# Kernel optimization log

Hardware: AMD Instinct MI355X
Metric: run time of the kernel (lower is better)

## Reference

```python
import jax, jax.numpy as jnp
import numpy as np


def setup_inputs() -> dict:
    key = jax.random.key(0)
    k1, k2 = jax.random.split(key)
    B, D = 8192, 256
    z1 = jax.random.normal(k1, (B, D), dtype=jnp.float32)
    z2 = jax.random.normal(k2, (B, D), dtype=jnp.float32)
    temperature = 0.1
    logit_scale = jnp.asarray(np.log(1.0 / temperature), dtype=jnp.float32)
    return {"z1": z1, "z2": z2, "logit_scale": logit_scale}


def reference(z1, z2, logit_scale):
    B = z1.shape[0]
    z = jnp.concatenate([z1, z2], axis=0)            # [2B, D]
    scale = jnp.minimum(jnp.exp(logit_scale), 100.0)
    logits = jnp.matmul(z, z.T) * scale              # [2B, 2B]
    N = 2 * B
    eye = jnp.eye(N, dtype=bool)
    logits = jnp.where(eye, jnp.float32(-1e9), logits)
    targets = jnp.concatenate([jnp.arange(B, 2 * B), jnp.arange(0, B)], axis=0)
    logp = jax.nn.log_softmax(logits, axis=-1)       # stable single-pass
    nll = -jnp.take_along_axis(logp, targets[:, None], axis=-1)[:, 0]
    return jnp.mean(nll)
```

## Files before the change

kernel.cpp:

```cpp
#include <hip/hip_runtime.h>
#include <hip/hip_bf16.h>

#define N_TOT 16384
#define B_HALF 8192
#define D 256
#define NGRAN 32
#define BN 32
#define NSPLIT 8
#define COLS_PER_SPLIT (N_TOT / NSPLIT)
#define NTILES (COLS_PER_SPLIT / BN)
#define NWAVE 8
#define BM (NWAVE * 64)

#define LOG2E 1.4426950408889634f
#define LN2   0.6931471805599453f

typedef short bf16x8 __attribute__((ext_vector_type(8)));
typedef float f32x4 __attribute__((ext_vector_type(4)));

__device__ __forceinline__ float fexp2(float x) {
#if __has_builtin(__builtin_amdgcn_exp2f)
    return __builtin_amdgcn_exp2f(x);
#else
    return __expf(x * LN2);
#endif
}

__device__ __forceinline__ ushort f2bf(float x) {
    uint32_t u = __float_as_uint(x);
    uint32_t r = u + 0x7FFFu + ((u >> 16) & 1u);
    return (ushort)(r >> 16);
}

__global__ void convert_kernel(const float* __restrict__ z1,
                               const float* __restrict__ z2,
                               const float* __restrict__ lsp,
                               ushort* __restrict__ zt) {
    const float scale = fminf(__expf(lsp[0]), 100.0f);
    const float s = __fsqrt_rn(scale * LOG2E);
    int T = blockIdx.x * blockDim.x + threadIdx.x;
    const int c = T >> 14;
    const int r = T & (N_TOT - 1);
    const int half_elems = B_HALF * D;
    int e = r * D + c * 8;
    const float* src = (e < half_elems) ? (z1 + e) : (z2 + (e - half_elems));
    float4 f0 = *reinterpret_cast<const float4*>(src);
    float4 f1 = *reinterpret_cast<const float4*>(src + 4);
    ushort o[8];
    o[0] = f2bf(f0.x * s); o[1] = f2bf(f0.y * s); o[2] = f2bf(f0.z * s); o[3] = f2bf(f0.w * s);
    o[4] = f2bf(f1.x * s); o[5] = f2bf(f1.y * s); o[6] = f2bf(f1.z * s); o[7] = f2bf(f1.w * s);
    *reinterpret_cast<bf16x8*>(zt + (size_t)T * 8) = *reinterpret_cast<bf16x8*>(o);
}

__global__ void target_kernel(const float* __restrict__ z1,
                              const float* __restrict__ z2,
                              const float* __restrict__ lsp,
                              float* __restrict__ tnat) {
    const int r    = blockIdx.x * 4 + (threadIdx.x >> 6);
    const int lane = threadIdx.x & 63;
    const float* zr = (r < B_HALF) ? (z1 + (size_t)r * D) : (z2 + (size_t)(r - B_HALF) * D);
    const float* zp = (r < B_HALF) ? (z2 + (size_t)r * D) : (z1 + (size_t)(r - B_HALF) * D);
    float4 a = *reinterpret_cast<const float4*>(zr + lane * 4);
    float4 b = *reinterpret_cast<const float4*>(zp + lane * 4);
    float d = a.x * b.x + a.y * b.y + a.z * b.z + a.w * b.w;
#pragma unroll
    for (int off = 1; off < 64; off <<= 1) d += __shfl_xor(d, off);
    if (lane == 0) {
        const float scale = fminf(__expf(lsp[0]), 100.0f);
        tnat[r] = scale * d;
    }
}

template<bool MASKD>
__device__ __forceinline__ void epilogue(const f32x4 (&acc)[4][2],
                                         float (&m2)[16], float (&l2)[16],
                                         int qrow0, int crow0, int g, int lg) {
#pragma unroll
    for (int mi = 0; mi < 4; ++mi) {
#pragma unroll
        for (int j = 0; j < 4; ++j) {
            const int slot = mi * 4 + j;
            float v0 = acc[mi][0][j], v1 = acc[mi][1][j];
            if (MASKD) {
                const int r  = qrow0 + mi * 16 + g * 4 + j;
                const int c0 = crow0 + lg;
                if (c0      == r) v0 = -1e30f;
                if (c0 + 16 == r) v1 = -1e30f;
            }
            const float m_old = m2[slot];
            float m_new = fmaxf(fmaxf(v0, v1), m_old);
            float er = fexp2(m_old - m_new);
            float e0 = fexp2(v0 - m_new);
            float e1 = fexp2(v1 - m_new);
            l2[slot] = __builtin_fmaf(l2[slot], er, e0 + e1);
            m2[slot] = m_new;
        }
    }
}

__global__ __launch_bounds__(512)
__attribute__((amdgpu_waves_per_eu(2, 2)))
void infonce_main(const ushort* __restrict__ zt,
                  float* __restrict__ part) {
    __shared__ ushort ks[NWAVE][BN * NGRAN * 8];

    const int tid  = threadIdx.x;
    const int wid  = tid >> 6;
    const int lane = tid & 63;
    const int g    = lane >> 4;
    const int lg   = lane & 15;
    const int qrow0   = blockIdx.y * BM + wid * 64;
    const int split   = blockIdx.x;
    const int colbase = split * COLS_PER_SPLIT;

    bf16x8 afrag[4][8];
#pragma unroll
    for (int kk = 0; kk < 8; ++kk)
#pragma unroll
        for (int mi = 0; mi < 4; ++mi)
            afrag[mi][kk] = *reinterpret_cast<const bf16x8*>(
                zt + ((size_t)(kk * 4 + g) * N_TOT + qrow0 + mi * 16 + lg) * 8);

    float m2[16], l2[16];
#pragma unroll
    for (int s = 0; s < 16; ++s) { m2[s] = -1e30f; l2[s] = 0.0f; }

    const ushort* srcW = zt + ((size_t)(lane >> 5) * N_TOT + (lane & 31)) * 8;

#define STAGE(t)                                                                     \
    {                                                                                \
        const ushort* s_ = srcW + (size_t)(colbase + (t) * BN) * 8;                  \
        _Pragma("unroll")                                                            \
        for (int it = 0; it < 16; ++it)                                              \
            __builtin_amdgcn_global_load_lds(                                        \
                (const __attribute__((address_space(1))) void*)(s_ + (size_t)it * 2 * N_TOT * 8), \
                (__attribute__((address_space(3))) void*)&ks[wid][it * 512],         \
                16, 0, 0);                                                           \
    }

    if (wid & 4) __builtin_amdgcn_s_sleep(19);

    STAGE(0);

    const char* kb = (const char*)(&ks[wid][0]) + g * 512 + lg * 16;

    for (int t = 0; t < NTILES; ++t) {
        asm volatile("s_waitcnt vmcnt(0)" ::: "memory");
        __builtin_amdgcn_sched_barrier(0);

        f32x4 acc[4][2];
#pragma unroll
        for (int mi = 0; mi < 4; ++mi)
#pragma unroll
            for (int n = 0; n < 2; ++n) acc[mi][n] = (f32x4){0.f, 0.f, 0.f, 0.f};

#pragma unroll
        for (int kk = 0; kk < 8; ++kk) {
#pragma unroll
            for (int n = 0; n < 2; ++n) {
                bf16x8 b = *reinterpret_cast<const bf16x8*>(kb + kk * 2048 + n * 256);
                acc[0][n] = __builtin_amdgcn_mfma_f32_16x16x32_bf16(afrag[0][kk], b, acc[0][n], 0, 0, 0);
                acc[1][n] = __builtin_amdgcn_mfma_f32_16x16x32_bf16(afrag[1][kk], b, acc[1][n], 0, 0, 0);
                acc[2][n] = __builtin_amdgcn_mfma_f32_16x16x32_bf16(afrag[2][kk], b, acc[2][n], 0, 0, 0);
                acc[3][n] = __builtin_amdgcn_mfma_f32_16x16x32_bf16(afrag[3][kk], b, acc[3][n], 0, 0, 0);
            }
        }

        asm volatile("s_waitcnt lgkmcnt(0)" ::: "memory");
        __builtin_amdgcn_sched_barrier(0);
        if (t + 1 < NTILES) STAGE(t + 1);

        const int crow0 = colbase + t * BN;
        if ((crow0 >> 6) == (qrow0 >> 6))
            epilogue<true >(acc, m2, l2, qrow0, crow0, g, lg);
        else
            epilogue<false>(acc, m2, l2, qrow0, crow0, g, lg);
    }
#undef STAGE

#pragma unroll
    for (int s = 0; s < 16; ++s) {
        float m = m2[s], l = l2[s];
#pragma unroll
        for (int off = 1; off < 16; off <<= 1) {
            float mo = __shfl_xor(m, off);
            float lo = __shfl_xor(l, off);
            float mm = fmaxf(m, mo);
            l = l * fexp2(m - mm) + lo * fexp2(mo - mm);
            m = mm;
        }
        m2[s] = m; l2[s] = l;
    }
    if (lg == 0) {
#pragma unroll
        for (int mi = 0; mi < 4; ++mi)
#pragma unroll
            for (int j = 0; j < 4; ++j) {
                int r = qrow0 + mi * 16 + g * 4 + j;
                int s = mi * 4 + j;
                float* p = part + (size_t)(r * NSPLIT + split) * 2;
                p[0] = m2[s]; p[1] = l2[s];
            }
    }
}

__global__ void reduce_kernel(const float* __restrict__ part,
                              const float* __restrict__ tnat,
                              float* __restrict__ bsum) {
    int r = blockIdx.x * 256 + threadIdx.x;
    float m = -1e30f, l = 0.f;
#pragma unroll
    for (int s = 0; s < NSPLIT; ++s) {
        const float* p = part + (size_t)(r * NSPLIT + s) * 2;
        float ms = p[0], lv = p[1];
        float mm = fmaxf(m, ms);
        l = l * fexp2(m - mm) + lv * fexp2(ms - mm);
        m = mm;
    }
    float v = LN2 * (m + __log2f(l)) - tnat[r];
#pragma unroll
    for (int off = 1; off < 64; off <<= 1) v += __shfl_xor(v, off);
    __shared__ float ws4[4];
    int lane = threadIdx.x & 63, wid = threadIdx.x >> 6;
    if (lane == 0) ws4[wid] = v;
    __syncthreads();
    if (threadIdx.x == 0)
        bsum[blockIdx.x] = ws4[0] + ws4[1] + ws4[2] + ws4[3];
}

__global__ void final_kernel(const float* __restrict__ bsum,
                             float* __restrict__ out) {
    float v = bsum[threadIdx.x];
#pragma unroll
    for (int off = 1; off < 64; off <<= 1) v += __shfl_xor(v, off);
    if (threadIdx.x == 0) out[0] = v * (1.0f / (float)N_TOT);
}

extern "C" void kernel_launch(void* const* d_in, const int* in_sizes, int n_in,
                              void* d_out, int out_size, void* d_ws, size_t ws_size,
                              hipStream_t stream) {
    const float* z1 = (const float*)d_in[0];
    const float* z2 = (const float*)d_in[1];
    const float* ls = (const float*)d_in[2];
    float* out = (float*)d_out;

    ushort* zt   = (ushort*)d_ws;
    float*  part = (float*)((char*)d_ws + (size_t)N_TOT * D * 2);
    float*  tnat = (float*)((char*)part + (size_t)N_TOT * NSPLIT * 2 * sizeof(float));
    float*  bsum = (float*)((char*)tnat + (size_t)N_TOT * sizeof(float));

    convert_kernel<<<(N_TOT * NGRAN) / 256, 256, 0, stream>>>(z1, z2, ls, zt);
    target_kernel<<<N_TOT / 4, 256, 0, stream>>>(z1, z2, ls, tnat);
    dim3 grid(NSPLIT, N_TOT / BM);
    infonce_main<<<grid, 512, 0, stream>>>(zt, part);
    reduce_kernel<<<N_TOT / 256, 256, 0, stream>>>(part, tnat, bsum);
    final_kernel<<<1, 64, 0, stream>>>(bsum, out);
}
```

Baseline: 158.4 us.

## Software-pipeline MFMA tiles with previous tile's softmax epilogue via double accumulators

```diff
diff --git a/kernel.cpp b/kernel.cpp
--- a/kernel.cpp
+++ b/kernel.cpp
@@ -71,12 +71,12 @@
     }
 }
 
-template<bool MASKD>
-__device__ __forceinline__ void epilogue(const f32x4 (&acc)[4][2],
+template<bool MASKD, int MI0>
+__device__ __forceinline__ void epi_half(const f32x4 (&acc)[4][2],
                                          float (&m2)[16], float (&l2)[16],
                                          int qrow0, int crow0, int g, int lg) {
 #pragma unroll
-    for (int mi = 0; mi < 4; ++mi) {
+    for (int mi = MI0; mi < MI0 + 2; ++mi) {
 #pragma unroll
         for (int j = 0; j < 4; ++j) {
             const int slot = mi * 4 + j;
@@ -138,44 +138,75 @@
                 16, 0, 0);                                                           \
     }
 
-    if (wid & 4) __builtin_amdgcn_s_sleep(19);
+    const char* kb = (const char*)(&ks[wid][0]) + g * 512 + lg * 16;
+
+    f32x4 accA[4][2], accB[4][2];
+
+#define ZERO(ACC)                                                                    \
+    { _Pragma("unroll") for (int mi = 0; mi < 4; ++mi)                               \
+        _Pragma("unroll") for (int n = 0; n < 2; ++n)                                \
+            ACC[mi][n] = (f32x4){0.f, 0.f, 0.f, 0.f}; }
+
+#define MFMA_HALF(ACC, KK0)                                                          \
+    { _Pragma("unroll") for (int kk = KK0; kk < (KK0) + 4; ++kk) {                   \
+        _Pragma("unroll") for (int n = 0; n < 2; ++n) {                              \
+            bf16x8 b = *reinterpret_cast<const bf16x8*>(kb + kk * 2048 + n * 256);   \
+            ACC[0][n] = __builtin_amdgcn_mfma_f32_16x16x32_bf16(afrag[0][kk], b, ACC[0][n], 0, 0, 0); \
+            ACC[1][n] = __builtin_amdgcn_mfma_f32_16x16x32_bf16(afrag[1][kk], b, ACC[1][n], 0, 0, 0); \
+            ACC[2][n] = __builtin_amdgcn_mfma_f32_16x16x32_bf16(afrag[2][kk], b, ACC[2][n], 0, 0, 0); \
+            ACC[3][n] = __builtin_amdgcn_mfma_f32_16x16x32_bf16(afrag[3][kk], b, ACC[3][n], 0, 0, 0); \
+        } } }
+
+#define EPI_H0(ACCE, CROW)                                                           \
+    { if (((CROW) >> 6) == (qrow0 >> 6)) epi_half<true , 0>(ACCE, m2, l2, qrow0, (CROW), g, lg); \
+      else                               epi_half<false, 0>(ACCE, m2, l2, qrow0, (CROW), g, lg); }
+#define EPI_H1(ACCE, CROW)                                                           \
+    { if (((CROW) >> 6) == (qrow0 >> 6)) epi_half<true , 2>(ACCE, m2, l2, qrow0, (CROW), g, lg); \
+      else                               epi_half<false, 2>(ACCE, m2, l2, qrow0, (CROW), g, lg); }
+
+#define BODY(T, ACCW, ACCE)                                                          \
+    {                                                                                \
+        const int crow_prev = colbase + ((T) - 1) * BN;                              \
+        asm volatile("s_waitcnt vmcnt(0)" ::: "memory");        \
+        __builtin_amdgcn_sched_barrier(0);                                           \
+        ZERO(ACCW);                                                                  \
+        __builtin_amdgcn_s_setprio(1);                                               \
+        MFMA_HALF(ACCW, 0);                                                          \
+        EPI_H0(ACCE, crow_prev);                           \
+        MFMA_HALF(ACCW, 4);                                                          \
+        __builtin_amdgcn_s_setprio(0);                                               \
+        asm volatile("s_waitcnt lgkmcnt(0)" ::: "memory");        \
+        __builtin_amdgcn_sched_barrier(0);                                           \
+        if ((T) + 1 < NTILES) STAGE((T) + 1);                                        \
+        EPI_H1(ACCE, crow_prev);                            \
+    }
 
     STAGE(0);
-
-    const char* kb = (const char*)(&ks[wid][0]) + g * 512 + lg * 16;
-
-    for (int t = 0; t < NTILES; ++t) {
-        asm volatile("s_waitcnt vmcnt(0)" ::: "memory");
-        __builtin_amdgcn_sched_barrier(0);
-
-        f32x4 acc[4][2];
-#pragma unroll
-        for (int mi = 0; mi < 4; ++mi)
-#pragma unroll
-            for (int n = 0; n < 2; ++n) acc[mi][n] = (f32x4){0.f, 0.f, 0.f, 0.f};
-
-#pragma unroll
-        for (int kk = 0; kk < 8; ++kk) {
-#pragma unroll
-            for (int n = 0; n < 2; ++n) {
-                bf16x8 b = *reinterpret_cast<const bf16x8*>(kb + kk * 2048 + n * 256);
-                acc[0][n] = __builtin_amdgcn_mfma_f32_16x16x32_bf16(afrag[0][kk], b, acc[0][n], 0, 0, 0);
-                acc[1][n] = __builtin_amdgcn_mfma_f32_16x16x32_bf16(afrag[1][kk], b, acc[1][n], 0, 0, 0);
-                acc[2][n] = __builtin_amdgcn_mfma_f32_16x16x32_bf16(afrag[2][kk], b, acc[2][n], 0, 0, 0);
-                acc[3][n] = __builtin_amdgcn_mfma_f32_16x16x32_bf16(afrag[3][kk], b, acc[3][n], 0, 0, 0);
-            }
-        }
-
-        asm volatile("s_waitcnt lgkmcnt(0)" ::: "memory");
-        __builtin_amdgcn_sched_barrier(0);
-        if (t + 1 < NTILES) STAGE(t + 1);
-
-        const int crow0 = colbase + t * BN;
-        if ((crow0 >> 6) == (qrow0 >> 6))
-            epilogue<true >(acc, m2, l2, qrow0, crow0, g, lg);
-        else
-            epilogue<false>(acc, m2, l2, qrow0, crow0, g, lg);
-    }
+    asm volatile("s_waitcnt vmcnt(0)" ::: "memory");
+    __builtin_amdgcn_sched_barrier(0);
+    ZERO(accB);
+    MFMA_HALF(accB, 0);
+    MFMA_HALF(accB, 4);
+    asm volatile("s_waitcnt lgkmcnt(0)" ::: "memory");
+    __builtin_amdgcn_sched_barrier(0);
+    STAGE(1);
+
+    for (int tp = 0; tp < 31; ++tp) {
+        BODY(2 * tp + 1, accA, accB);
+        BODY(2 * tp + 2, accB, accA);
+    }
+    BODY(63, accA, accB);
+
+    {
+        const int crow_last = colbase + 63 * BN;
+        EPI_H0(accA, crow_last);
+        EPI_H1(accA, crow_last);
+    }
+#undef BODY
+#undef EPI_H0
+#undef EPI_H1
+#undef MFMA_HALF
+#undef ZERO
 #undef STAGE
 
 #pragma unroll
```

Result: slower. 168.3 us (+6.3%).

## Gate online-softmax exp updates per wave and split load wait across K halves

Applied to the files above, without the earlier changes.

```diff
diff --git a/kernel.cpp b/kernel.cpp
--- a/kernel.cpp
+++ b/kernel.cpp
@@ -14,6 +14,7 @@
 
 #define LOG2E 1.4426950408889634f
 #define LN2   0.6931471805599453f
+#define GATE_THR 30.0f
 
 typedef short bf16x8 __attribute__((ext_vector_type(8)));
 typedef float f32x4 __attribute__((ext_vector_type(4)));
@@ -72,28 +73,39 @@
 }
 
 template<bool MASKD>
-__device__ __forceinline__ void epilogue(const f32x4 (&acc)[4][2],
-                                         float (&m2)[16], float (&l2)[16],
-                                         int qrow0, int crow0, int g, int lg) {
+__device__ __forceinline__ void epilogue_g(const f32x4 (&acc)[4][2],
+                                           float (&m2)[16], float (&l2)[16],
+                                           int qrow0, int crow0, int g, int lg) {
 #pragma unroll
     for (int mi = 0; mi < 4; ++mi) {
-#pragma unroll
-        for (int j = 0; j < 4; ++j) {
-            const int slot = mi * 4 + j;
-            float v0 = acc[mi][0][j], v1 = acc[mi][1][j];
-            if (MASKD) {
-                const int r  = qrow0 + mi * 16 + g * 4 + j;
-                const int c0 = crow0 + lg;
-                if (c0      == r) v0 = -1e30f;
-                if (c0 + 16 == r) v1 = -1e30f;
-            }
-            const float m_old = m2[slot];
-            float m_new = fmaxf(fmaxf(v0, v1), m_old);
-            float er = fexp2(m_old - m_new);
-            float e0 = fexp2(v0 - m_new);
-            float e1 = fexp2(v1 - m_new);
-            l2[slot] = __builtin_fmaf(l2[slot], er, e0 + e1);
-            m2[slot] = m_new;
+        float v0[4], v1[4];
+#pragma unroll
+        for (int j = 0; j < 4; ++j) { v0[j] = acc[mi][0][j]; v1[j] = acc[mi][1][j]; }
+        if (MASKD) {
+            const int c0 = crow0 + lg;
+#pragma unroll
+            for (int j = 0; j < 4; ++j) {
+                const int r = qrow0 + mi * 16 + g * 4 + j;
+                if (c0      == r) v0[j] = -1e30f;
+                if (c0 + 16 == r) v1[j] = -1e30f;
+            }
+        }
+        const int s0 = mi * 4;
+        float gmax = fmaxf(fmaxf(fmaxf(v0[0], v1[0]), fmaxf(v0[1], v1[1])),
+                           fmaxf(fmaxf(v0[2], v1[2]), fmaxf(v0[3], v1[3])));
+        float mmin = fminf(fminf(m2[s0], m2[s0 + 1]), fminf(m2[s0 + 2], m2[s0 + 3]));
+        if (__any(gmax > mmin - GATE_THR)) {
+#pragma unroll
+            for (int j = 0; j < 4; ++j) {
+                const int slot = s0 + j;
+                const float m_old = m2[slot];
+                float m_new = fmaxf(fmaxf(v0[j], v1[j]), m_old);
+                float er = fexp2(m_old - m_new);
+                float e0 = fexp2(v0[j] - m_new);
+                float e1 = fexp2(v1[j] - m_new);
+                l2[slot] = __builtin_fmaf(l2[slot], er, e0 + e1);
+                m2[slot] = m_new;
+            }
         }
     }
 }
@@ -145,17 +157,16 @@
     const char* kb = (const char*)(&ks[wid][0]) + g * 512 + lg * 16;
 
     for (int t = 0; t < NTILES; ++t) {
-        asm volatile("s_waitcnt vmcnt(0)" ::: "memory");
+        f32x4 acc[4][2];
+#pragma unroll
+        for (int mi = 0; mi < 4; ++mi)
+#pragma unroll
+            for (int n = 0; n < 2; ++n) acc[mi][n] = (f32x4){0.f, 0.f, 0.f, 0.f};
+
+        asm volatile("s_waitcnt vmcnt(8)" ::: "memory");
         __builtin_amdgcn_sched_barrier(0);
-
-        f32x4 acc[4][2];
-#pragma unroll
-        for (int mi = 0; mi < 4; ++mi)
-#pragma unroll
-            for (int n = 0; n < 2; ++n) acc[mi][n] = (f32x4){0.f, 0.f, 0.f, 0.f};
-
-#pragma unroll
-        for (int kk = 0; kk < 8; ++kk) {
+#pragma unroll
+        for (int kk = 0; kk < 4; ++kk) {
 #pragma unroll
             for (int n = 0; n < 2; ++n) {
                 bf16x8 b = *reinterpret_cast<const bf16x8*>(kb + kk * 2048 + n * 256);
@@ -165,6 +176,19 @@
                 acc[3][n] = __builtin_amdgcn_mfma_f32_16x16x32_bf16(afrag[3][kk], b, acc[3][n], 0, 0, 0);
             }
         }
+        asm volatile("s_waitcnt vmcnt(0)" ::: "memory");
+        __builtin_amdgcn_sched_barrier(0);
+#pragma unroll
+        for (int kk = 4; kk < 8; ++kk) {
+#pragma unroll
+            for (int n = 0; n < 2; ++n) {
+                bf16x8 b = *reinterpret_cast<const bf16x8*>(kb + kk * 2048 + n * 256);
+                acc[0][n] = __builtin_amdgcn_mfma_f32_16x16x32_bf16(afrag[0][kk], b, acc[0][n], 0, 0, 0);
+                acc[1][n] = __builtin_amdgcn_mfma_f32_16x16x32_bf16(afrag[1][kk], b, acc[1][n], 0, 0, 0);
+                acc[2][n] = __builtin_amdgcn_mfma_f32_16x16x32_bf16(afrag[2][kk], b, acc[2][n], 0, 0, 0);
+                acc[3][n] = __builtin_amdgcn_mfma_f32_16x16x32_bf16(afrag[3][kk], b, acc[3][n], 0, 0, 0);
+            }
+        }
 
         asm volatile("s_waitcnt lgkmcnt(0)" ::: "memory");
         __builtin_amdgcn_sched_barrier(0);
@@ -172,9 +196,9 @@
 
         const int crow0 = colbase + t * BN;
         if ((crow0 >> 6) == (qrow0 >> 6))
-            epilogue<true >(acc, m2, l2, qrow0, crow0, g, lg);
+            epilogue_g<true >(acc, m2, l2, qrow0, crow0, g, lg);
         else
-            epilogue<false>(acc, m2, l2, qrow0, crow0, g, lg);
+            epilogue_g<false>(acc, m2, l2, qrow0, crow0, g, lg);
     }
 #undef STAGE
 
```

New measurement: 239.6 us. 1.51x slower.

## Split waves into MFMA producers and softmax consumers with shared double buffers

Applied to the files above, without the earlier changes.

```diff
diff --git a/kernel.cpp b/kernel.cpp
--- a/kernel.cpp
+++ b/kernel.cpp
@@ -6,17 +6,21 @@
 #define D 256
 #define NGRAN 32
 #define BN 32
-#define NSPLIT 8
+#define NSPLIT 4
 #define COLS_PER_SPLIT (N_TOT / NSPLIT)
-#define NTILES (COLS_PER_SPLIT / BN)
-#define NWAVE 8
-#define BM (NWAVE * 64)
+#define NT (COLS_PER_SPLIT / BN)
+#define BM 256
 
 #define LOG2E 1.4426950408889634f
 #define LN2   0.6931471805599453f
 
 typedef short bf16x8 __attribute__((ext_vector_type(8)));
 typedef float f32x4 __attribute__((ext_vector_type(4)));
+
+#define SBAR() asm volatile("s_barrier" ::: "memory")
+#define WAITV4()   { asm volatile("s_waitcnt vmcnt(4)" ::: "memory"); __builtin_amdgcn_sched_barrier(0); }
+#define WAITV0()   { asm volatile("s_waitcnt vmcnt(0)" ::: "memory"); __builtin_amdgcn_sched_barrier(0); }
+#define WAITLGKM() { asm volatile("s_waitcnt lgkmcnt(0)" ::: "memory"); __builtin_amdgcn_sched_barrier(0); }
 
 __device__ __forceinline__ float fexp2(float x) {
 #if __has_builtin(__builtin_amdgcn_exp2f)
@@ -102,105 +106,131 @@
 __attribute__((amdgpu_waves_per_eu(2, 2)))
 void infonce_main(const ushort* __restrict__ zt,
                   float* __restrict__ part) {
-    __shared__ ushort ks[NWAVE][BN * NGRAN * 8];
+    __shared__ ushort ks[2][BN * NGRAN * 8];
+    __shared__ float  accb[2][4][2048];
 
     const int tid  = threadIdx.x;
     const int wid  = tid >> 6;
     const int lane = tid & 63;
     const int g    = lane >> 4;
     const int lg   = lane & 15;
-    const int qrow0   = blockIdx.y * BM + wid * 64;
-    const int split   = blockIdx.x;
-    const int colbase = split * COLS_PER_SPLIT;
-
-    bf16x8 afrag[4][8];
-#pragma unroll
-    for (int kk = 0; kk < 8; ++kk)
-#pragma unroll
-        for (int mi = 0; mi < 4; ++mi)
-            afrag[mi][kk] = *reinterpret_cast<const bf16x8*>(
-                zt + ((size_t)(kk * 4 + g) * N_TOT + qrow0 + mi * 16 + lg) * 8);
-
-    float m2[16], l2[16];
-#pragma unroll
-    for (int s = 0; s < 16; ++s) { m2[s] = -1e30f; l2[s] = 0.0f; }
-
-    const ushort* srcW = zt + ((size_t)(lane >> 5) * N_TOT + (lane & 31)) * 8;
-
-#define STAGE(t)                                                                     \
-    {                                                                                \
-        const ushort* s_ = srcW + (size_t)(colbase + (t) * BN) * 8;                  \
-        _Pragma("unroll")                                                            \
-        for (int it = 0; it < 16; ++it)                                              \
-            __builtin_amdgcn_global_load_lds(                                        \
-                (const __attribute__((address_space(1))) void*)(s_ + (size_t)it * 2 * N_TOT * 8), \
-                (__attribute__((address_space(3))) void*)&ks[wid][it * 512],         \
-                16, 0, 0);                                                           \
-    }
-
-    if (wid & 4) __builtin_amdgcn_s_sleep(19);
-
-    STAGE(0);
-
-    const char* kb = (const char*)(&ks[wid][0]) + g * 512 + lg * 16;
-
-    for (int t = 0; t < NTILES; ++t) {
-        asm volatile("s_waitcnt vmcnt(0)" ::: "memory");
-        __builtin_amdgcn_sched_barrier(0);
-
-        f32x4 acc[4][2];
-#pragma unroll
-        for (int mi = 0; mi < 4; ++mi)
-#pragma unroll
-            for (int n = 0; n < 2; ++n) acc[mi][n] = (f32x4){0.f, 0.f, 0.f, 0.f};
-
-#pragma unroll
-        for (int kk = 0; kk < 8; ++kk) {
-#pragma unroll
-            for (int n = 0; n < 2; ++n) {
-                bf16x8 b = *reinterpret_cast<const bf16x8*>(kb + kk * 2048 + n * 256);
-                acc[0][n] = __builtin_amdgcn_mfma_f32_16x16x32_bf16(afrag[0][kk], b, acc[0][n], 0, 0, 0);
-                acc[1][n] = __builtin_amdgcn_mfma_f32_16x16x32_bf16(afrag[1][kk], b, acc[1][n], 0, 0, 0);
-                acc[2][n] = __builtin_amdgcn_mfma_f32_16x16x32_bf16(afrag[2][kk], b, acc[2][n], 0, 0, 0);
-                acc[3][n] = __builtin_amdgcn_mfma_f32_16x16x32_bf16(afrag[3][kk], b, acc[3][n], 0, 0, 0);
-            }
-        }
-
-        asm volatile("s_waitcnt lgkmcnt(0)" ::: "memory");
-        __builtin_amdgcn_sched_barrier(0);
-        if (t + 1 < NTILES) STAGE(t + 1);
-
-        const int crow0 = colbase + t * BN;
-        if ((crow0 >> 6) == (qrow0 >> 6))
-            epilogue<true >(acc, m2, l2, qrow0, crow0, g, lg);
-        else
-            epilogue<false>(acc, m2, l2, qrow0, crow0, g, lg);
-    }
+    const bool isProd = (wid < 4);
+    const int band  = isProd ? wid : (wid - 4);
+    const int qrow0 = blockIdx.y * BM + band * 64;
+    const int colbase = blockIdx.x * COLS_PER_SPLIT;
+
+    const int accoff = g * 128 + lg * 4;
+
+    if (isProd) {
+        bf16x8 afrag[4][8];
+#pragma unroll
+        for (int kk = 0; kk < 8; ++kk)
+#pragma unroll
+            for (int mi = 0; mi < 4; ++mi)
+                afrag[mi][kk] = *reinterpret_cast<const bf16x8*>(
+                    zt + ((size_t)(kk * 4 + g) * N_TOT + qrow0 + mi * 16 + lg) * 8);
+
+        const ushort* srcW = zt + ((size_t)(wid * 2 + (lane >> 5)) * N_TOT + (lane & 31)) * 8;
+        const int dstbase = (wid * 64) * 8;
+
+#define STAGE(buf, t)                                                               \
+    {                                                                               \
+        const ushort* s_ = srcW + (size_t)(colbase + (t) * BN) * 8;                 \
+        _Pragma("unroll")                                                           \
+        for (int it = 0; it < 4; ++it)                                              \
+            __builtin_amdgcn_global_load_lds(                                       \
+                (const __attribute__((address_space(1))) void*)(s_ + (size_t)it * 8 * N_TOT * 8), \
+                (__attribute__((address_space(3))) void*)&ks[buf][it * 2048 + dstbase], \
+                16, 0, 0);                                                          \
+    }
+
+        const char* kb0 = (const char*)(&ks[0][0]) + g * 512 + lg * 16;
+
+        STAGE(0, 0);
+
+        for (int t = 0; t <= NT; ++t) {
+            SBAR();
+            if (t < NT) {
+                if (t + 1 < NT) { STAGE((t + 1) & 1, t + 1); WAITV4(); }
+                else            { WAITV0(); }
+
+                f32x4 acc[4][2];
+#pragma unroll
+                for (int mi = 0; mi < 4; ++mi)
+#pragma unroll
+                    for (int n = 0; n < 2; ++n) acc[mi][n] = (f32x4){0.f, 0.f, 0.f, 0.f};
+
+                const char* kb = kb0 + ((t & 1) << 14);
+#pragma unroll
+                for (int kk = 0; kk < 8; ++kk) {
+#pragma unroll
+                    for (int n = 0; n < 2; ++n) {
+                        bf16x8 b = *reinterpret_cast<const bf16x8*>(kb + kk * 2048 + n * 256);
+                        acc[0][n] = __builtin_amdgcn_mfma_f32_16x16x32_bf16(afrag[0][kk], b, acc[0][n], 0, 0, 0);
+                        acc[1][n] = __builtin_amdgcn_mfma_f32_16x16x32_bf16(afrag[1][kk], b, acc[1][n], 0, 0, 0);
+                        acc[2][n] = __builtin_amdgcn_mfma_f32_16x16x32_bf16(afrag[2][kk], b, acc[2][n], 0, 0, 0);
+                        acc[3][n] = __builtin_amdgcn_mfma_f32_16x16x32_bf16(afrag[3][kk], b, acc[3][n], 0, 0, 0);
+                    }
+                }
+
+                float* ab = &accb[t & 1][band][0] + accoff;
+#pragma unroll
+                for (int mi = 0; mi < 4; ++mi)
+#pragma unroll
+                    for (int n = 0; n < 2; ++n)
+                        *reinterpret_cast<f32x4*>(ab + mi * 512 + n * 64) = acc[mi][n];
+                WAITLGKM();
+            }
+        }
 #undef STAGE
-
-#pragma unroll
-    for (int s = 0; s < 16; ++s) {
-        float m = m2[s], l = l2[s];
-#pragma unroll
-        for (int off = 1; off < 16; off <<= 1) {
-            float mo = __shfl_xor(m, off);
-            float lo = __shfl_xor(l, off);
-            float mm = fmaxf(m, mo);
-            l = l * fexp2(m - mm) + lo * fexp2(mo - mm);
-            m = mm;
-        }
-        m2[s] = m; l2[s] = l;
-    }
-    if (lg == 0) {
-#pragma unroll
-        for (int mi = 0; mi < 4; ++mi)
-#pragma unroll
-            for (int j = 0; j < 4; ++j) {
-                int r = qrow0 + mi * 16 + g * 4 + j;
-                int s = mi * 4 + j;
-                float* p = part + (size_t)(r * NSPLIT + split) * 2;
-                p[0] = m2[s]; p[1] = l2[s];
-            }
+    } else {
+        float m2[16], l2[16];
+#pragma unroll
+        for (int s = 0; s < 16; ++s) { m2[s] = -1e30f; l2[s] = 0.0f; }
+
+        for (int t = 0; t <= NT; ++t) {
+            SBAR();
+            if (t > 0) {
+                const float* ab = &accb[(t - 1) & 1][band][0] + accoff;
+                f32x4 acc[4][2];
+#pragma unroll
+                for (int mi = 0; mi < 4; ++mi)
+#pragma unroll
+                    for (int n = 0; n < 2; ++n)
+                        acc[mi][n] = *reinterpret_cast<const f32x4*>(ab + mi * 512 + n * 64);
+
+                const int crow0 = colbase + (t - 1) * BN;
+                if ((crow0 >> 6) == (qrow0 >> 6))
+                    epilogue<true >(acc, m2, l2, qrow0, crow0, g, lg);
+                else
+                    epilogue<false>(acc, m2, l2, qrow0, crow0, g, lg);
+            }
+        }
+
+#pragma unroll
+        for (int s = 0; s < 16; ++s) {
+            float m = m2[s], l = l2[s];
+#pragma unroll
+            for (int off = 1; off < 16; off <<= 1) {
+                float mo = __shfl_xor(m, off);
+                float lo = __shfl_xor(l, off);
+                float mm = fmaxf(m, mo);
+                l = l * fexp2(m - mm) + lo * fexp2(mo - mm);
+                m = mm;
+            }
+            m2[s] = m; l2[s] = l;
+        }
+        if (lg == 0) {
+#pragma unroll
+            for (int mi = 0; mi < 4; ++mi)
+#pragma unroll
+                for (int j = 0; j < 4; ++j) {
+                    int r = qrow0 + mi * 16 + g * 4 + j;
+                    int s = mi * 4 + j;
+                    float* p = part + (size_t)(r * NSPLIT + blockIdx.x) * 2;
+                    p[0] = m2[s]; p[1] = l2[s];
+                }
+        }
     }
 }
 
```

New measurement: 203.4 us. 28.4% more time.
